# Kernel optimization log

Hardware: AMD Instinct MI355X
Metric: run time of the kernel (lower is better)

The kernel has to match this reference:

```python
import jax, jax.numpy as jnp
import numpy as np

D_MODEL = 96
D_EXP = 192      # d_expand == d_inner (ssm_ratio=ssm_rank_ratio=2)
D_STATE = 16
DT_RANK = 6      # ceil(96/16)
DC_IN = 4        # dc_inner
DC_STATE = 16
DTC_RANK = 6
B, H, W = 2, 48, 48


def _ln_channel(x, w, b):
    # WithBias LayerNorm over channel dim (torch code reshapes b c h w -> b (hw) c)
    mu = x.mean(axis=1, keepdims=True)
    var = ((x - mu) ** 2).mean(axis=1, keepdims=True)
    return (x - mu) / jnp.sqrt(var + 1e-5) * w[None, :, None, None] + b[None, :, None, None]


def _selective_scan(u, delta, A, Bs, Cs, D, delta_bias):
    # u, delta: (b,k,d,l); A: (k,d,n); Bs,Cs: (b,k,n,l); D, delta_bias: (k,d)
    delta = jax.nn.softplus(delta + delta_bias[None, :, :, None])
    dA = jnp.exp(jnp.einsum('bkdl,kdn->bkldn', delta, A))          # decay per step
    dBu = jnp.einsum('bkdl,bkdl,bknl->bkldn', delta, u, Bs)        # input injection

    def combine(c1, c2):
        a1, b1 = c1
        a2, b2 = c2
        return a1 * a2, a2 * b1 + b2

    _, hs = jax.lax.associative_scan(combine, (dA, dBu), axis=2)   # parallel linear recurrence over l
    return jnp.einsum('bkldn,bknl->bkdl', hs, Cs) + D[None, :, :, None] * u


def _spatial_core(x, x_proj_w, dt_w, dt_b, A_logs, Ds, onw, onb):
    b, d, h, w = x.shape
    l = h * w
    # cross_scan_2d: row-major, col-major, and their flips -> (b,4,d,l)
    xs = jnp.stack([x.reshape(b, d, l), jnp.swapaxes(x, 2, 3).reshape(b, d, l)], 1)
    xs = jnp.concatenate([xs, jnp.flip(xs, -1)], 1)
    x_dbl = jnp.einsum('bkdl,kcd->bkcl', xs, x_proj_w)
    dts, Bs, Cs = jnp.split(x_dbl, [DT_RANK, DT_RANK + D_STATE], axis=2)
    dts = jnp.einsum('bkrl,kdr->bkdl', dts, dt_w)
    A = -jnp.exp(A_logs).reshape(4, d, D_STATE)
    out_y = _selective_scan(xs, dts, A, Bs, Cs, Ds.reshape(4, d), dt_b)  # (b,4,d,l)
    inv = jnp.flip(out_y[:, 2:4], -1)
    wh = jnp.swapaxes(out_y[:, 1].reshape(b, d, w, h), 2, 3).reshape(b, d, l)
    invwh = jnp.swapaxes(inv[:, 1].reshape(b, d, w, h), 2, 3).reshape(b, d, l)
    y = (out_y[:, 0] + inv[:, 0] + wh + invwh).reshape(b, d, h, w)
    return _ln_channel(y, onw, onb)


def _channel_core(y, cin_w, cin_b, cout_w, cout_b, xc_proj_w, dtc_w, dtc_b, Ac_logs, Dsc, cnw, cnb):
    b, d = y.shape[0], y.shape[1]
    xc = y.mean(axis=(2, 3))                                              # adaptive avg pool -> (b,d)
    xc = xc[:, None, :] * cin_w.reshape(1, DC_IN, 1) + cin_b.reshape(1, DC_IN, 1)  # 1x1 conv_cin -> (b,4,d)
    xsc = jnp.stack([xc, jnp.flip(xc, -1)], 1)                            # (b,2,dc,L=d)
    xc_dbl = jnp.einsum('bkdl,kcd->bkcl', xsc, xc_proj_w)
    dtsc, Bc, Cc = jnp.split(xc_dbl, [DTC_RANK, DTC_RANK + DC_STATE], axis=2)
    dtsc = jnp.einsum('bkrl,kdr->bkdl', dtsc, dtc_w)
    Ac = -jnp.exp(Ac_logs).reshape(2, DC_IN, DC_STATE)
    outc = _selective_scan(xsc, dtsc, Ac, Bc, Cc, Dsc.reshape(2, DC_IN), dtc_b)  # (b,2,dc,d)
    yc = outc[:, 0] + jnp.flip(outc[:, 1], -1)                            # merge fwd/bwd channel scans
    yc = jnp.einsum('bdl,d->bl', yc, cout_w.reshape(DC_IN)) + cout_b.reshape(())  # 1x1 conv_cout
    return _ln_channel(yc.reshape(b, d, 1, 1), cnw, cnb)


def _conv1x1(x, w, b):
    return jnp.einsum('bchw,oc->bohw', x, w.reshape(w.shape[0], w.shape[1])) + b[None, :, None, None]


def _forward(x, in_w, in_b, dw_w, dw_b, x_proj_w, dt_w, dt_b, A_logs, Ds, out_norm_w, out_norm_b,
             cin_w, cin_b, cout_w, cout_b, xc_proj_w, dtc_w, dtc_b, Ac_logs, Dsc, cn_w, cn_b,
             out_w, out_b):
    xz = _conv1x1(x, in_w, in_b)                      # (b, 2*d_expand, h, w)
    x1, z = xz[:, :D_EXP], xz[:, D_EXP:]
    z = jax.nn.silu(z)
    x1 = jax.lax.conv_general_dilated(x1, dw_w, (1, 1), 'SAME',
                                      dimension_numbers=('NCHW', 'OIHW', 'NCHW'),
                                      feature_group_count=D_EXP) + dw_b[None, :, None, None]
    x1 = jax.nn.silu(x1)
    y = _spatial_core(x1, x_proj_w, dt_w, dt_b, A_logs, Ds, out_norm_w, out_norm_b)
    c = _channel_core(y, cin_w, cin_b, cout_w, cout_b, xc_proj_w, dtc_w, dtc_b, Ac_logs, Dsc, cn_w, cn_b)
    y = y * c * z                                     # channel modulation + gating
    return _conv1x1(y, out_w, out_b)


def setup_inputs():
    key = jax.random.key(0)
    ks = jax.random.split(key, 24)
    s = 0.02

    def rn(k, shape, scale=s):
        return jax.random.normal(k, shape, jnp.float32) * scale

    A_logs = jnp.log(jnp.tile(jnp.arange(1, D_STATE + 1, dtype=jnp.float32)[None, :], (4 * D_EXP, 1)))
    return dict(
        x=jax.random.normal(ks[0], (B, D_MODEL, H, W), jnp.float32),
        in_w=rn(ks[1], (2 * D_EXP, D_MODEL, 1, 1)),
        in_b=rn(ks[2], (2 * D_EXP,)),
        dw_w=rn(ks[3], (D_EXP, 1, 3, 3)),
        dw_b=rn(ks[4], (D_EXP,)),
        x_proj_w=rn(ks[5], (4, DT_RANK + 2 * D_STATE, D_EXP)),
        dt_w=rn(ks[6], (4, D_EXP, DT_RANK), 0.1),
        dt_b=rn(ks[7], (4, D_EXP), 0.5) - 4.0,
        A_logs=A_logs,
        Ds=jnp.ones((4 * D_EXP,), jnp.float32),
        out_norm_w=jnp.ones((D_EXP,), jnp.float32),
        out_norm_b=jnp.zeros((D_EXP,), jnp.float32),
        cin_w=rn(ks[8], (DC_IN, 1, 1, 1), 0.5),
        cin_b=rn(ks[9], (DC_IN,), 0.1),
        cout_w=rn(ks[10], (1, DC_IN, 1, 1), 0.5),
        cout_b=rn(ks[11], (1,), 0.1),
        xc_proj_w=rn(ks[12], (2, DTC_RANK + 2 * DC_STATE, DC_IN), 0.2),
        dtc_w=rn(ks[13], (2, DC_IN, DTC_RANK), 0.2),
        dtc_b=rn(ks[14], (2, DC_IN), 0.5),
        Ac_logs=rn(ks[15], (2 * DC_IN, DC_STATE), 1.0),
        Dsc=jnp.ones((2 * DC_IN,), jnp.float32),
        cn_w=jnp.ones((D_EXP,), jnp.float32),
        cn_b=jnp.zeros((D_EXP,), jnp.float32),
        out_w=rn(ks[16], (D_MODEL, D_EXP, 1, 1)),
        out_b=rn(ks[17], (D_MODEL,)),
    )


def reference(x, in_w, in_b, dw_w, dw_b, x_proj_w, dt_w, dt_b, A_logs, Ds, out_norm_w, out_norm_b,
              cin_w, cin_b, cout_w, cout_b, xc_proj_w, dtc_w, dtc_b, Ac_logs, Dsc, cn_w, cn_b,
              out_w, out_b):
    return _forward(x, in_w, in_b, dw_w, dw_b, x_proj_w, dt_w, dt_b, A_logs, Ds, out_norm_w, out_norm_b,
                    cin_w, cin_b, cout_w, cout_b, xc_proj_w, dtc_w, dtc_b, Ac_logs, Dsc, cn_w, cn_b,
                    out_w, out_b)
```

## Files before the change

### kernel.cpp

```cpp
#include <hip/hip_runtime.h>
#include <math.h>

#define DM 96
#define DE 192
#define LL 2304
#define NS 16
#define RK 6
#define NC 38
#define CH4 64
#define CL4 36

__device__ __forceinline__ float silu_f(float x){ return x / (1.f + __expf(-x)); }
__device__ __forceinline__ float softplus_f(float x){
  return (x > 20.f) ? x : __logf(1.f + __expf(x));
}

__device__ __forceinline__ int dir_map(int k, int l){
    switch(k){
      case 0: return l;
      case 1: return (l % 48) * 48 + l / 48;
      case 2: return 2303 - l;
      default: { int lr = 2303 - l; return (lr % 48) * 48 + lr / 48; }
    }
}

__global__ __launch_bounds__(384) void k1_conv_in(const float* __restrict__ x,
    const float* __restrict__ in_w, const float* __restrict__ in_b,
    float* __restrict__ x1raw, float* __restrict__ z){
  __shared__ float xv[DM*16];
  int tile = blockIdx.x;
  int b = tile / 144;
  int pos0 = (tile % 144) * 16;
  int tid = threadIdx.x;
  {
    int c = tid >> 2, p4 = tid & 3;
    float4 v = *(const float4*)(x + (b*DM + c)*LL + pos0 + p4*4);
    *(float4*)&xv[c*16 + p4*4] = v;
  }
  __syncthreads();
  float acc[16];
  #pragma unroll
  for (int p=0;p<16;p++) acc[p] = in_b[tid];
  const float4* wv4 = (const float4*)(in_w + tid*DM);
  #pragma unroll 4
  for (int c4=0;c4<24;c4++){
    float4 wv = wv4[c4];
    #pragma unroll
    for (int cc=0;cc<4;cc++){
      float w = (cc==0)?wv.x:((cc==1)?wv.y:((cc==2)?wv.z:wv.w));
      const float* xr = &xv[(c4*4+cc)*16];
      #pragma unroll
      for (int p4=0;p4<4;p4++){
        float4 xq = *(const float4*)&xr[p4*4];
        acc[p4*4+0] = fmaf(w, xq.x, acc[p4*4+0]);
        acc[p4*4+1] = fmaf(w, xq.y, acc[p4*4+1]);
        acc[p4*4+2] = fmaf(w, xq.z, acc[p4*4+2]);
        acc[p4*4+3] = fmaf(w, xq.w, acc[p4*4+3]);
      }
    }
  }
  if (tid < DE){
    float* dst = x1raw + (b*DE + tid)*LL + pos0;
    #pragma unroll
    for (int p4=0;p4<4;p4++)
      *(float4*)(dst + p4*4) = make_float4(acc[p4*4+0],acc[p4*4+1],acc[p4*4+2],acc[p4*4+3]);
  } else {
    int zc = tid - DE;
    float* dst = z + (b*DE + zc)*LL + pos0;
    #pragma unroll
    for (int p4=0;p4<4;p4++)
      *(float4*)(dst + p4*4) = make_float4(silu_f(acc[p4*4+0]),silu_f(acc[p4*4+1]),
                                           silu_f(acc[p4*4+2]),silu_f(acc[p4*4+3]));
  }
}

__global__ __launch_bounds__(256) void k2_dwconv(const float* __restrict__ x1raw,
    const float* __restrict__ dw_w, const float* __restrict__ dw_b,
    float* __restrict__ xconv, float* __restrict__ xconvT){
  __shared__ float lin[50][52];
  __shared__ float lout[48][50];
  int bd = blockIdx.x;
  int d = bd % DE;
  int tid = threadIdx.x;
  for (int i = tid; i < 50*52; i += 256) ((float*)lin)[i] = 0.f;
  __syncthreads();
  const float* src = x1raw + bd*LL;
  for (int i = tid; i < 576; i += 256){
    int r = i/12, c4 = (i%12)*4;
    float4 v = *(const float4*)(src + r*48 + c4);
    lin[r+1][c4+1] = v.x; lin[r+1][c4+2] = v.y; lin[r+1][c4+3] = v.z; lin[r+1][c4+4] = v.w;
  }
  float w00=dw_w[d*9+0], w01=dw_w[d*9+1], w02=dw_w[d*9+2];
  float w10=dw_w[d*9+3], w11=dw_w[d*9+4], w12=dw_w[d*9+5];
  float w20=dw_w[d*9+6], w21=dw_w[d*9+7], w22=dw_w[d*9+8];
  float bias = dw_b[d];
  __syncthreads();
  float* dst = xconv + bd*LL;
  for (int i = tid; i < 576; i += 256){
    int h = i/12, w4 = (i%12)*4;
    float o[4];
    #pragma unroll
    for (int j=0;j<4;j++){
      int w = w4 + j;
      float acc = bias;
      acc = fmaf(w00, lin[h  ][w], fmaf(w01, lin[h  ][w+1], fmaf(w02, lin[h  ][w+2], acc)));
      acc = fmaf(w10, lin[h+1][w], fmaf(w11, lin[h+1][w+1], fmaf(w12, lin[h+1][w+2], acc)));
      acc = fmaf(w20, lin[h+2][w], fmaf(w21, lin[h+2][w+1], fmaf(w22, lin[h+2][w+2], acc)));
      float v = silu_f(acc);
      o[j] = v;
      lout[h][w] = v;
    }
    *(float4*)(dst + h*48 + w4) = make_float4(o[0],o[1],o[2],o[3]);
  }
  __syncthreads();
  float* dstT = xconvT + bd*LL;
  for (int i = tid; i < 576; i += 256){
    int tw = i/12, th4 = (i%12)*4;
    float4 v = make_float4(lout[th4][tw], lout[th4+1][tw], lout[th4+2][tw], lout[th4+3][tw]);
    *(float4*)(dstT + tw*48 + th4) = v;
  }
}

__global__ __launch_bounds__(256) void k3_proj(const float* __restrict__ xconv,
    const float* __restrict__ xconvT,
    const float* __restrict__ x_proj_w, const float* __restrict__ dt_w,
    const float* __restrict__ dt_b, float* __restrict__ delta,
    float* __restrict__ Bs, float* __restrict__ Cs){
  __shared__ float smem[38*256];
  int bk = blockIdx.x / 36;
  int tile = blockIdx.x % 36;
  int b = bk >> 2, k = bk & 3;
  int tid = threadIdx.x;
  int lsub = tid & 63, dgrp = tid >> 6;
  int l = tile*64 + lsub;
  const float* wsrc = x_proj_w + k*NC*DE;
  for (int idx = tid; idx < NC*DE; idx += 256){
    int c = idx / DE, d = idx % DE;
    smem[d*40 + c] = wsrc[idx];
  }
  if (tid < DE){ smem[tid*40 + 38] = 0.f; smem[tid*40 + 39] = 0.f; }
  __syncthreads();
  float acc[40];
  #pragma unroll
  for (int c=0;c<40;c++) acc[c]=0.f;
  const float* uptr;
  {
    const float* basep = (k & 1) ? (xconvT + b*DE*LL) : (xconv + b*DE*LL);
    uptr = basep + ((k >= 2) ? (2303 - l) : l);
  }
  for (int dd=0; dd<48; dd++){
    int d = dgrp*48 + dd;
    float u = uptr[d*LL];
    const float4* wrow = (const float4*)&smem[d*40];
    #pragma unroll
    for (int j=0;j<10;j++){
      float4 wv = wrow[j];
      acc[j*4+0] = fmaf(u, wv.x, acc[j*4+0]);
      acc[j*4+1] = fmaf(u, wv.y, acc[j*4+1]);
      acc[j*4+2] = fmaf(u, wv.z, acc[j*4+2]);
      acc[j*4+3] = fmaf(u, wv.w, acc[j*4+3]);
    }
  }
  __syncthreads();
  #pragma unroll
  for (int c=0;c<38;c++) smem[c*256 + dgrp*64 + lsub] = acc[c];
  __syncthreads();
  for (int idx = tid; idx < 38*64; idx += 256){
    int c = idx >> 6, l2 = idx & 63;
    float s = smem[c*256 + l2] + smem[c*256 + 64 + l2]
            + smem[c*256 + 128 + l2] + smem[c*256 + 192 + l2];
    int lg = tile*64 + l2;
    if (c < RK){
      smem[c*256 + l2] = s;
    } else if (c < RK + NS){
      Bs[(bk*LL + lg)*NS + (c - RK)] = s;
    } else {
      Cs[(bk*LL + lg)*NS + (c - RK - NS)] = s;
    }
  }
  __syncthreads();
  float r0 = smem[0*256 + lsub], r1 = smem[1*256 + lsub], r2 = smem[2*256 + lsub];
  float r3 = smem[3*256 + lsub], r4 = smem[4*256 + lsub], r5 = smem[5*256 + lsub];
  const float* dwb = dt_w + k*DE*RK;
  const float* dbb = dt_b + k*DE;
  for (int dd=0; dd<48; dd++){
    int d = dgrp*48 + dd;
    const float* wr = dwb + d*RK;
    float t = dbb[d];
    t = fmaf(r0, wr[0], t); t = fmaf(r1, wr[1], t); t = fmaf(r2, wr[2], t);
    t = fmaf(r3, wr[3], t); t = fmaf(r4, wr[4], t); t = fmaf(r5, wr[5], t);
    delta[(bk*DE + d)*LL + l] = softplus_f(t);
  }
}

__global__ __launch_bounds__(256) void k4_scan(const float* __restrict__ xconv,
    const float* __restrict__ xconvT,
    const float* __restrict__ delta, const float* __restrict__ Bs,
    const float* __restrict__ Cs, const float* __restrict__ A_logs,
    const float* __restrict__ Ds, float* __restrict__ out_y){
  int gid = blockIdx.x;
  int b = gid / (4*DE);
  int kd = gid % (4*DE);
  int k = kd / DE;
  int d = kd % DE;
  int bk = b*4 + k;
  int tid = threadIdx.x;
  int c = tid >> 2, q = tid & 3;
  const float LOG2E = 1.44269504f;
  float4 al = *(const float4*)&A_logs[(k*DE + d)*NS + q*4];
  float A2[4];
  A2[0] = -__expf(al.x)*LOG2E; A2[1] = -__expf(al.y)*LOG2E;
  A2[2] = -__expf(al.z)*LOG2E; A2[3] = -__expf(al.w)*LOG2E;
  float Dv = Ds[k*DE + d];
  const float* dptr = delta + (bk*DE + d)*LL;
  const float* ub = ((k & 1) ? xconvT : xconv) + (b*DE + d)*LL;
  bool rev = (k >= 2);
  const float* bbase = Bs + bk*LL*NS + q*4;
  const float* cbase = Cs + bk*LL*NS + q*4;
  float* optr = out_y + (bk*DE + d)*LL;
  int l0 = c*CL4;
  float sumdl = 0.f, S[4] = {0.f,0.f,0.f,0.f};
  #pragma unroll 3
  for (int i=0;i<CL4;i+=4){
    int l = l0 + i;
    float4 dl4 = *(const float4*)(dptr + l);
    float4 u4;
    if (!rev) u4 = *(const float4*)(ub + l);
    else { float4 t = *(const float4*)(ub + (LL-4) - l); u4 = make_float4(t.w,t.z,t.y,t.x); }
    #pragma unroll
    for (int j=0;j<4;j++){
      float dlj = (j==0)?dl4.x:((j==1)?dl4.y:((j==2)?dl4.z:dl4.w));
      float uj  = (j==0)?u4.x:((j==1)?u4.y:((j==2)?u4.z:u4.w));
      float du = dlj*uj;
      sumdl += dlj;
      float4 Bv = *(const float4*)(bbase + (l+j)*NS);
      float dA0 = exp2f(dlj*A2[0]); S[0] = fmaf(S[0], dA0, du*Bv.x);
      float dA1 = exp2f(dlj*A2[1]); S[1] = fmaf(S[1], dA1, du*Bv.y);
      float dA2 = exp2f(dlj*A2[2]); S[2] = fmaf(S[2], dA2, du*Bv.z);
      float dA3 = exp2f(dlj*A2[3]); S[3] = fmaf(S[3], dA3, du*Bv.w);
    }
  }
  __shared__ float sP[CH4][NS], sS[CH4][NS];
  __shared__ float oy[LL];
  *(float4*)&sP[c][q*4] = make_float4(exp2f(A2[0]*sumdl), exp2f(A2[1]*sumdl),
                                      exp2f(A2[2]*sumdl), exp2f(A2[3]*sumdl));
  *(float4*)&sS[c][q*4] = make_float4(S[0],S[1],S[2],S[3]);
  __syncthreads();
  if (tid < NS){
    float hacc = 0.f;
    #pragma unroll 4
    for (int cc=0; cc<CH4; cc++){
      hacc = fmaf(hacc, sP[cc][tid], sS[cc][tid]);
      sS[cc][tid] = hacc;
    }
  }
  __syncthreads();
  float h[4];
  if (c == 0){ h[0]=h[1]=h[2]=h[3]=0.f; }
  else { float4 hi = *(const float4*)&sS[c-1][q*4]; h[0]=hi.x; h[1]=hi.y; h[2]=hi.z; h[3]=hi.w; }
  #pragma unroll 3
  for (int i=0;i<CL4;i+=4){
    int l = l0 + i;
    float4 dl4 = *(const float4*)(dptr + l);
    float4 u4;
    if (!rev) u4 = *(const float4*)(ub + l);
    else { float4 t = *(const float4*)(ub + (LL-4) - l); u4 = make_float4(t.w,t.z,t.y,t.x); }
    #pragma unroll
    for (int j=0;j<4;j++){
      float dlj = (j==0)?dl4.x:((j==1)?dl4.y:((j==2)?dl4.z:dl4.w));
      float uj  = (j==0)?u4.x:((j==1)?u4.y:((j==2)?u4.z:u4.w));
      float du = dlj*uj;
      float4 Bv = *(const float4*)(bbase + (l+j)*NS);
      float4 Cv = *(const float4*)(cbase + (l+j)*NS);
      float dA0 = exp2f(dlj*A2[0]); h[0] = fmaf(h[0], dA0, du*Bv.x);
      float dA1 = exp2f(dlj*A2[1]); h[1] = fmaf(h[1], dA1, du*Bv.y);
      float dA2 = exp2f(dlj*A2[2]); h[2] = fmaf(h[2], dA2, du*Bv.z);
      float dA3 = exp2f(dlj*A2[3]); h[3] = fmaf(h[3], dA3, du*Bv.w);
      float py = h[0]*Cv.x + h[1]*Cv.y + h[2]*Cv.z + h[3]*Cv.w;
      py += __shfl_xor(py, 1);
      py += __shfl_xor(py, 2);
      if (q == 0){
        oy[dir_map(k, l+j)] = fmaf(Dv, uj, py);
      }
    }
  }
  __syncthreads();
  {
    float4* o4 = (float4*)optr;
    const float4* s4 = (const float4*)oy;
    for (int i = tid; i < LL/4; i += 256) o4[i] = s4[i];
  }
}

__global__ __launch_bounds__(256) void k5_combine_ln(const float* __restrict__ out_y,
    const float* __restrict__ onw, const float* __restrict__ onb,
    float* __restrict__ y_ln, float* __restrict__ partial){
  __shared__ float vals[DE][17];
  __shared__ float s_[16][16], s2_[16][16];
  __shared__ float mu_[16], rs_[16];
  int bT = blockIdx.x;
  int b = bT / 144;
  int pos0 = (bT % 144) * 16;
  int tid = threadIdx.x;
  int p = tid & 15, g = tid >> 4;
  const float* base = out_y + b*4*DE*LL;
  float s = 0.f, s2 = 0.f;
  #pragma unroll
  for (int j=0;j<12;j++){
    int d = g*12 + j;
    int idx = d*LL + pos0 + p;
    float v = base[idx] + base[DE*LL + idx] + base[2*DE*LL + idx] + base[3*DE*LL + idx];
    vals[d][p] = v;
    s += v; s2 += v*v;
  }
  s_[g][p] = s; s2_[g][p] = s2;
  __syncthreads();
  if (tid < 16){
    float ss = 0.f, ss2 = 0.f;
    #pragma unroll
    for (int gg=0; gg<16; gg++){ ss += s_[gg][tid]; ss2 += s2_[gg][tid]; }
    float mu = ss / DE;
    float var = ss2 / DE - mu*mu;
    mu_[tid] = mu; rs_[tid] = rsqrtf(var + 1e-5f);
  }
  __syncthreads();
  float mu = mu_[p], rs = rs_[p];
  #pragma unroll
  for (int j=0;j<12;j++){
    int d = g*12 + j;
    float yv = (vals[d][p] - mu)*rs*onw[d] + onb[d];
    y_ln[(b*DE + d)*LL + pos0 + p] = yv;
    vals[d][p] = yv;
  }
  __syncthreads();
  if (tid < DE){
    float ps = 0.f;
    #pragma unroll
    for (int pp=0;pp<16;pp++) ps += vals[tid][pp];
    partial[bT*DE + tid] = ps;
  }
}

__global__ __launch_bounds__(512) void k6b_channel(const float* __restrict__ partial,
    const float* __restrict__ cin_w, const float* __restrict__ cin_b,
    const float* __restrict__ cout_w, const float* __restrict__ cout_b,
    const float* __restrict__ xc_proj_w, const float* __restrict__ dtc_w,
    const float* __restrict__ dtc_b, const float* __restrict__ Ac_logs,
    const float* __restrict__ Dsc, const float* __restrict__ cn_w,
    const float* __restrict__ cn_b, float* __restrict__ cvec){
  __shared__ float xcs[DE];
  __shared__ float tmp[384];
  __shared__ float sP[128][4], sS[128][4];
  __shared__ float outc[2][4][DE];
  __shared__ float ycs[DE];
  __shared__ float muS, rsS;
  int b = blockIdx.x;
  int tid = threadIdx.x;
  if (tid < 384){
    int d = tid % DE, half = tid / DE;
    const float* pp = partial + (b*144 + half*72)*DE + d;
    float sacc = 0.f;
    #pragma unroll 8
    for (int t=0;t<72;t++) sacc += pp[t*DE];
    tmp[tid] = sacc;
  }
  __syncthreads();
  if (tid < DE) xcs[tid] = (tmp[tid] + tmp[tid + DE]) * (1.f/LL);
  __syncthreads();
  int chain = tid >> 2, ch = tid & 3;
  int k = chain >> 6, dc = (chain >> 4) & 3, n = chain & 15;
  const float LOG2E = 1.44269504f;
  float EW0=0,EW1=0,EW2=0,EW3=0;
  #pragma unroll
  for (int r=0;r<RK;r++){
    float dw = dtc_w[(k*4+dc)*RK + r];
    EW0 = fmaf(dw, xc_proj_w[(k*NC + r)*4 + 0], EW0);
    EW1 = fmaf(dw, xc_proj_w[(k*NC + r)*4 + 1], EW1);
    EW2 = fmaf(dw, xc_proj_w[(k*NC + r)*4 + 2], EW2);
    EW3 = fmaf(dw, xc_proj_w[(k*NC + r)*4 + 3], EW3);
  }
  float Bw0 = xc_proj_w[(k*NC + RK + n)*4 + 0];
  float Bw1 = xc_proj_w[(k*NC + RK + n)*4 + 1];
  float Bw2 = xc_proj_w[(k*NC + RK + n)*4 + 2];
  float Bw3 = xc_proj_w[(k*NC + RK + n)*4 + 3];
  float Cw0 = xc_proj_w[(k*NC + RK + NS + n)*4 + 0];
  float Cw1 = xc_proj_w[(k*NC + RK + NS + n)*4 + 1];
  float Cw2 = xc_proj_w[(k*NC + RK + NS + n)*4 + 2];
  float Cw3 = xc_proj_w[(k*NC + RK + NS + n)*4 + 3];
  float A2 = -__expf(Ac_logs[(k*4+dc)*NS + n]) * LOG2E;
  float Dv = Dsc[k*4+dc];
  float dtb = dtc_b[k*4+dc];
  float ciw0=cin_w[0], ciw1=cin_w[1], ciw2=cin_w[2], ciw3=cin_w[3];
  float cib0=cin_b[0], cib1=cin_b[1], cib2=cin_b[2], cib3=cin_b[3];
  int l0 = ch*48;
  float P = 1.f, S = 0.f;
  for (int i=0;i<48;i++){
    int lc = l0 + i;
    int lp = k ? (191 - lc) : lc;
    float xv = xcs[lp];
    float xs0 = fmaf(xv, ciw0, cib0);
    float xs1 = fmaf(xv, ciw1, cib1);
    float xs2 = fmaf(xv, ciw2, cib2);
    float xs3 = fmaf(xv, ciw3, cib3);
    float dt = dtb + xs0*EW0 + xs1*EW1 + xs2*EW2 + xs3*EW3;
    float dl = softplus_f(dt);
    float Bv = xs0*Bw0 + xs1*Bw1 + xs2*Bw2 + xs3*Bw3;
    float u = (dc==0)?xs0:((dc==1)?xs1:((dc==2)?xs2:xs3));
    float dA = exp2f(dl * A2);
    S = fmaf(S, dA, dl*u*Bv);
    P *= dA;
  }
  sP[chain][ch] = P; sS[chain][ch] = S;
  __syncthreads();
  if (tid < 128){
    float hacc = 0.f;
    #pragma unroll
    for (int cc=0; cc<4; cc++){
      hacc = fmaf(hacc, sP[tid][cc], sS[tid][cc]);
      sS[tid][cc] = hacc;
    }
  }
  __syncthreads();
  float h = (ch == 0) ? 0.f : sS[chain][ch-1];
  for (int i=0;i<48;i++){
    int lc = l0 + i;
    int lp = k ? (191 - lc) : lc;
    float xv = xcs[lp];
    float xs0 = fmaf(xv, ciw0, cib0);
    float xs1 = fmaf(xv, ciw1, cib1);
    float xs2 = fmaf(xv, ciw2, cib2);
    float xs3 = fmaf(xv, ciw3, cib3);
    float dt = dtb + xs0*EW0 + xs1*EW1 + xs2*EW2 + xs3*EW3;
    float dl = softplus_f(dt);
    float Bv = xs0*Bw0 + xs1*Bw1 + xs2*Bw2 + xs3*Bw3;
    float Cv = xs0*Cw0 + xs1*Cw1 + xs2*Cw2 + xs3*Cw3;
    float u = (dc==0)?xs0:((dc==1)?xs1:((dc==2)?xs2:xs3));
    float dA = exp2f(dl * A2);
    h = fmaf(h, dA, dl*u*Bv);
    float py = h * Cv;
    py += __shfl_xor(py, 4);
    py += __shfl_xor(py, 8);
    py += __shfl_xor(py, 16);
    py += __shfl_xor(py, 32);
    if (n == 0) outc[k][dc][lc] = fmaf(Dv, u, py);
  }
  __syncthreads();
  float co0=cout_w[0], co1=cout_w[1], co2=cout_w[2], co3=cout_w[3], cob=cout_b[0];
  for (int i = tid; i < DE; i += 512){
    float yv = cob
      + co0*(outc[0][0][i] + outc[1][0][191-i])
      + co1*(outc[0][1][i] + outc[1][1][191-i])
      + co2*(outc[0][2][i] + outc[1][2][191-i])
      + co3*(outc[0][3][i] + outc[1][3][191-i]);
    ycs[i] = yv;
  }
  __syncthreads();
  if (tid < 64){
    float s = 0.f, s2 = 0.f;
    #pragma unroll
    for (int j=0;j<3;j++){
      float v = ycs[tid + j*64];
      s += v; s2 += v*v;
    }
    for (int off=32; off>0; off>>=1){ s += __shfl_down(s, off); s2 += __shfl_down(s2, off); }
    if (tid == 0){
      float mu = s / DE;
      float var = s2 / DE - mu*mu;
      muS = mu; rsS = rsqrtf(var + 1e-5f);
    }
  }
  __syncthreads();
  float mu = muS, rs = rsS;
  for (int i = tid; i < DE; i += 512){
    cvec[b*DE + i] = (ycs[i] - mu) * rs * cn_w[i] + cn_b[i];
  }
}

__global__ __launch_bounds__(256) void k7_out(const float* __restrict__ y_ln,
    const float* __restrict__ cvec, const float* __restrict__ z,
    const float* __restrict__ out_w, const float* __restrict__ out_b,
    float* __restrict__ outp){
  __shared__ float t[DE*16];
  int tile = blockIdx.x;
  int b = tile / 144;
  int pos0 = (tile % 144) * 16;
  int tid = threadIdx.x;
  for (int i = tid; i < DE*4; i += 256){
    int c = i >> 2, p4 = (i & 3)*4;
    int gi = (b*DE + c)*LL + pos0 + p4;
    float4 yv = *(const float4*)(y_ln + gi);
    float4 zv = *(const float4*)(z + gi);
    float cv = cvec[b*DE + c];
    *(float4*)&t[c*16 + p4] = make_float4(yv.x*cv*zv.x, yv.y*cv*zv.y, yv.z*cv*zv.z, yv.w*cv*zv.w);
  }
  __syncthreads();
  for (int j = tid; j < DM*16; j += 256){
    int o = j >> 4, p = j & 15;
    float acc = out_b[o];
    const float4* wr4 = (const float4*)(out_w + o*DE);
    #pragma unroll 8
    for (int c4=0;c4<48;c4++){
      float4 wv = wr4[c4];
      acc = fmaf(wv.x, t[(c4*4+0)*16+p], acc);
      acc = fmaf(wv.y, t[(c4*4+1)*16+p], acc);
      acc = fmaf(wv.z, t[(c4*4+2)*16+p], acc);
      acc = fmaf(wv.w, t[(c4*4+3)*16+p], acc);
    }
    outp[(b*DM + o)*LL + pos0 + p] = acc;
  }
}

extern "C" void kernel_launch(void* const* d_in, const int* in_sizes, int n_in,
                              void* d_out, int out_size, void* d_ws, size_t ws_size,
                              hipStream_t stream){
  const float* x        = (const float*)d_in[0];
  const float* in_w     = (const float*)d_in[1];
  const float* in_b     = (const float*)d_in[2];
  const float* dw_w     = (const float*)d_in[3];
  const float* dw_b     = (const float*)d_in[4];
  const float* x_proj_w = (const float*)d_in[5];
  const float* dt_w     = (const float*)d_in[6];
  const float* dt_b     = (const float*)d_in[7];
  const float* A_logs   = (const float*)d_in[8];
  const float* Ds       = (const float*)d_in[9];
  const float* onw      = (const float*)d_in[10];
  const float* onb      = (const float*)d_in[11];
  const float* cin_w    = (const float*)d_in[12];
  const float* cin_b    = (const float*)d_in[13];
  const float* cout_w   = (const float*)d_in[14];
  const float* cout_b   = (const float*)d_in[15];
  const float* xc_proj_w= (const float*)d_in[16];
  const float* dtc_w    = (const float*)d_in[17];
  const float* dtc_b    = (const float*)d_in[18];
  const float* Ac_logs  = (const float*)d_in[19];
  const float* Dsc      = (const float*)d_in[20];
  const float* cn_w     = (const float*)d_in[21];
  const float* cn_b     = (const float*)d_in[22];
  const float* out_w    = (const float*)d_in[23];
  const float* out_b    = (const float*)d_in[24];

  float* ws = (float*)d_ws;
  float* x1raw = ws;  ws += 2*DE*LL;
  float* zbuf  = ws;  ws += 2*DE*LL;
  float* xconv = ws;  ws += 2*DE*LL;
  float* delta = ws;  ws += 2*4*DE*LL;
  float* Bsb   = ws;  ws += 2*4*LL*NS;
  float* Csb   = ws;  ws += 2*4*LL*NS;
  float* outy  = ws;  ws += 2*4*DE*LL;
  float* yln   = ws;  ws += 2*DE*LL;
  float* cvec  = ws;  ws += 2*DE;
  float* partial = ws; ws += 2*144*DE;
  float* xconvT = yln;

  hipLaunchKernelGGL(k1_conv_in, dim3(288), dim3(384), 0, stream, x, in_w, in_b, x1raw, zbuf);
  hipLaunchKernelGGL(k2_dwconv, dim3(384), dim3(256), 0, stream, x1raw, dw_w, dw_b, xconv, xconvT);
  hipLaunchKernelGGL(k3_proj, dim3(288), dim3(256), 0, stream, xconv, xconvT, x_proj_w, dt_w, dt_b, delta, Bsb, Csb);
  hipLaunchKernelGGL(k4_scan, dim3(1536), dim3(256), 0, stream, xconv, xconvT, delta, Bsb, Csb, A_logs, Ds, outy);
  hipLaunchKernelGGL(k5_combine_ln, dim3(288), dim3(256), 0, stream, outy, onw, onb, yln, partial);
  hipLaunchKernelGGL(k6b_channel, dim3(2), dim3(512), 0, stream, partial, cin_w, cin_b, cout_w, cout_b,
                     xc_proj_w, dtc_w, dtc_b, Ac_logs, Dsc, cn_w, cn_b, cvec);
  hipLaunchKernelGGL(k7_out, dim3(288), dim3(256), 0, stream, yln, cvec, zbuf, out_w, out_b, (float*)d_out);
}
```

Measured before the change: 185.6 us.

## Fuse four scan directions per block and defer LayerNorm apply to output kernel

The scan kernel now runs all four directions for one (batch, channel) in a single 1024-thread block and sums them in shared memory, writing one combined tensor instead of four per-direction outputs. The LayerNorm pass is split: a stats kernel writes per-position mean and rstd plus normalized partial sums, and the output projection kernel applies the norm inline. This cuts global traffic from writing and re-reading the four-direction out_y and the y_ln buffer. In exchange the scan uses larger blocks with 36KB of shared memory, which may lower occupancy, and adds an extra barrier.

```diff
diff --git a/kernel.cpp b/kernel.cpp
--- a/kernel.cpp
+++ b/kernel.cpp
@@ -193,19 +193,23 @@
   }
 }
 
-__global__ __launch_bounds__(256) void k4_scan(const float* __restrict__ xconv,
+__global__ __launch_bounds__(1024) void k4_scan(const float* __restrict__ xconv,
     const float* __restrict__ xconvT,
     const float* __restrict__ delta, const float* __restrict__ Bs,
     const float* __restrict__ Cs, const float* __restrict__ A_logs,
-    const float* __restrict__ Ds, float* __restrict__ out_y){
+    const float* __restrict__ Ds, float* __restrict__ ycomb){
+  __shared__ float smem4[4*LL];
+  float* sPf = smem4;
+  float* sSf = smem4 + 4096;
+  float* oyf = smem4;
   int gid = blockIdx.x;
-  int b = gid / (4*DE);
-  int kd = gid % (4*DE);
-  int k = kd / DE;
-  int d = kd % DE;
+  int b = gid / DE;
+  int d = gid % DE;
+  int tid = threadIdx.x;
+  int k = tid >> 8;
+  int sub = tid & 255;
+  int c = sub >> 2, q = sub & 3;
   int bk = b*4 + k;
-  int tid = threadIdx.x;
-  int c = tid >> 2, q = tid & 3;
   const float LOG2E = 1.44269504f;
   float4 al = *(const float4*)&A_logs[(k*DE + d)*NS + q*4];
   float A2[4];
@@ -217,7 +221,6 @@
   bool rev = (k >= 2);
   const float* bbase = Bs + bk*LL*NS + q*4;
   const float* cbase = Cs + bk*LL*NS + q*4;
-  float* optr = out_y + (bk*DE + d)*LL;
   int l0 = c*CL4;
   float sumdl = 0.f, S[4] = {0.f,0.f,0.f,0.f};
   #pragma unroll 3
@@ -240,24 +243,27 @@
       float dA3 = exp2f(dlj*A2[3]); S[3] = fmaf(S[3], dA3, du*Bv.w);
     }
   }
-  __shared__ float sP[CH4][NS], sS[CH4][NS];
-  __shared__ float oy[LL];
-  *(float4*)&sP[c][q*4] = make_float4(exp2f(A2[0]*sumdl), exp2f(A2[1]*sumdl),
-                                      exp2f(A2[2]*sumdl), exp2f(A2[3]*sumdl));
-  *(float4*)&sS[c][q*4] = make_float4(S[0],S[1],S[2],S[3]);
-  __syncthreads();
-  if (tid < NS){
+  *(float4*)&sPf[(k*CH4 + c)*NS + q*4] = make_float4(exp2f(A2[0]*sumdl), exp2f(A2[1]*sumdl),
+                                                     exp2f(A2[2]*sumdl), exp2f(A2[3]*sumdl));
+  *(float4*)&sSf[(k*CH4 + c)*NS + q*4] = make_float4(S[0],S[1],S[2],S[3]);
+  __syncthreads();
+  if (sub < NS){
     float hacc = 0.f;
     #pragma unroll 4
     for (int cc=0; cc<CH4; cc++){
-      hacc = fmaf(hacc, sP[cc][tid], sS[cc][tid]);
-      sS[cc][tid] = hacc;
+      int idx = (k*CH4 + cc)*NS + sub;
+      hacc = fmaf(hacc, sPf[idx], sSf[idx]);
+      sSf[idx] = hacc;
     }
   }
   __syncthreads();
   float h[4];
   if (c == 0){ h[0]=h[1]=h[2]=h[3]=0.f; }
-  else { float4 hi = *(const float4*)&sS[c-1][q*4]; h[0]=hi.x; h[1]=hi.y; h[2]=hi.z; h[3]=hi.w; }
+  else {
+    float4 hi = *(const float4*)&sSf[(k*CH4 + c-1)*NS + q*4];
+    h[0]=hi.x; h[1]=hi.y; h[2]=hi.z; h[3]=hi.w;
+  }
+  __syncthreads();
   #pragma unroll 3
   for (int i=0;i<CL4;i+=4){
     int l = l0 + i;
@@ -280,21 +286,28 @@
       py += __shfl_xor(py, 1);
       py += __shfl_xor(py, 2);
       if (q == 0){
-        oy[dir_map(k, l+j)] = fmaf(Dv, uj, py);
+        oyf[k*LL + dir_map(k, l+j)] = fmaf(Dv, uj, py);
       }
     }
   }
   __syncthreads();
   {
-    float4* o4 = (float4*)optr;
-    const float4* s4 = (const float4*)oy;
-    for (int i = tid; i < LL/4; i += 256) o4[i] = s4[i];
-  }
-}
-
-__global__ __launch_bounds__(256) void k5_combine_ln(const float* __restrict__ out_y,
-    const float* __restrict__ onw, const float* __restrict__ onb,
-    float* __restrict__ y_ln, float* __restrict__ partial){
+    float4* o4 = (float4*)(ycomb + (b*DE + d)*LL);
+    const float4* s0 = (const float4*)(oyf);
+    const float4* s1 = (const float4*)(oyf + LL);
+    const float4* s2 = (const float4*)(oyf + 2*LL);
+    const float4* s3 = (const float4*)(oyf + 3*LL);
+    for (int i = tid; i < LL/4; i += 1024){
+      float4 a = s0[i], e = s1[i], f = s2[i], g = s3[i];
+      o4[i] = make_float4(a.x+e.x+f.x+g.x, a.y+e.y+f.y+g.y,
+                          a.z+e.z+f.z+g.z, a.w+e.w+f.w+g.w);
+    }
+  }
+}
+
+__global__ __launch_bounds__(256) void k5_stats(const float* __restrict__ ycomb,
+    float* __restrict__ mu_g, float* __restrict__ rs_g,
+    float* __restrict__ partial){
   __shared__ float vals[DE][17];
   __shared__ float s_[16][16], s2_[16][16];
   __shared__ float mu_[16], rs_[16];
@@ -303,13 +316,12 @@
   int pos0 = (bT % 144) * 16;
   int tid = threadIdx.x;
   int p = tid & 15, g = tid >> 4;
-  const float* base = out_y + b*4*DE*LL;
+  const float* base = ycomb + b*DE*LL;
   float s = 0.f, s2 = 0.f;
   #pragma unroll
   for (int j=0;j<12;j++){
     int d = g*12 + j;
-    int idx = d*LL + pos0 + p;
-    float v = base[idx] + base[DE*LL + idx] + base[2*DE*LL + idx] + base[3*DE*LL + idx];
+    float v = base[d*LL + pos0 + p];
     vals[d][p] = v;
     s += v; s2 += v*v;
   }
@@ -322,26 +334,20 @@
     float mu = ss / DE;
     float var = ss2 / DE - mu*mu;
     mu_[tid] = mu; rs_[tid] = rsqrtf(var + 1e-5f);
-  }
-  __syncthreads();
-  float mu = mu_[p], rs = rs_[p];
-  #pragma unroll
-  for (int j=0;j<12;j++){
-    int d = g*12 + j;
-    float yv = (vals[d][p] - mu)*rs*onw[d] + onb[d];
-    y_ln[(b*DE + d)*LL + pos0 + p] = yv;
-    vals[d][p] = yv;
+    mu_g[b*LL + pos0 + tid] = mu;
+    rs_g[b*LL + pos0 + tid] = rs_[tid];
   }
   __syncthreads();
   if (tid < DE){
     float ps = 0.f;
     #pragma unroll
-    for (int pp=0;pp<16;pp++) ps += vals[tid][pp];
+    for (int pp=0;pp<16;pp++) ps += (vals[tid][pp] - mu_[pp]) * rs_[pp];
     partial[bT*DE + tid] = ps;
   }
 }
 
 __global__ __launch_bounds__(512) void k6b_channel(const float* __restrict__ partial,
+    const float* __restrict__ onw, const float* __restrict__ onb,
     const float* __restrict__ cin_w, const float* __restrict__ cin_b,
     const float* __restrict__ cout_w, const float* __restrict__ cout_b,
     const float* __restrict__ xc_proj_w, const float* __restrict__ dtc_w,
@@ -365,7 +371,7 @@
     tmp[tid] = sacc;
   }
   __syncthreads();
-  if (tid < DE) xcs[tid] = (tmp[tid] + tmp[tid + DE]) * (1.f/LL);
+  if (tid < DE) xcs[tid] = fmaf(onw[tid], (tmp[tid] + tmp[tid + DE]) * (1.f/LL), onb[tid]);
   __syncthreads();
   int chain = tid >> 2, ch = tid & 3;
   int k = chain >> 6, dc = (chain >> 4) & 3, n = chain & 15;
@@ -476,7 +482,9 @@
   }
 }
 
-__global__ __launch_bounds__(256) void k7_out(const float* __restrict__ y_ln,
+__global__ __launch_bounds__(256) void k7_out(const float* __restrict__ ycomb,
+    const float* __restrict__ mu_g, const float* __restrict__ rs_g,
+    const float* __restrict__ onw, const float* __restrict__ onb,
     const float* __restrict__ cvec, const float* __restrict__ z,
     const float* __restrict__ out_w, const float* __restrict__ out_b,
     float* __restrict__ outp){
@@ -488,10 +496,17 @@
   for (int i = tid; i < DE*4; i += 256){
     int c = i >> 2, p4 = (i & 3)*4;
     int gi = (b*DE + c)*LL + pos0 + p4;
-    float4 yv = *(const float4*)(y_ln + gi);
+    float4 yv = *(const float4*)(ycomb + gi);
     float4 zv = *(const float4*)(z + gi);
+    float4 m4 = *(const float4*)(mu_g + b*LL + pos0 + p4);
+    float4 r4 = *(const float4*)(rs_g + b*LL + pos0 + p4);
+    float w = onw[c], bb = onb[c];
     float cv = cvec[b*DE + c];
-    *(float4*)&t[c*16 + p4] = make_float4(yv.x*cv*zv.x, yv.y*cv*zv.y, yv.z*cv*zv.z, yv.w*cv*zv.w);
+    float t0 = fmaf((yv.x - m4.x)*r4.x, w, bb) * cv * zv.x;
+    float t1 = fmaf((yv.y - m4.y)*r4.y, w, bb) * cv * zv.y;
+    float t2 = fmaf((yv.z - m4.z)*r4.z, w, bb) * cv * zv.z;
+    float t3 = fmaf((yv.w - m4.w)*r4.w, w, bb) * cv * zv.w;
+    *(float4*)&t[c*16 + p4] = make_float4(t0,t1,t2,t3);
   }
   __syncthreads();
   for (int j = tid; j < DM*16; j += 256){
@@ -543,21 +558,22 @@
   float* x1raw = ws;  ws += 2*DE*LL;
   float* zbuf  = ws;  ws += 2*DE*LL;
   float* xconv = ws;  ws += 2*DE*LL;
+  float* xconvT= ws;  ws += 2*DE*LL;
   float* delta = ws;  ws += 2*4*DE*LL;
   float* Bsb   = ws;  ws += 2*4*LL*NS;
   float* Csb   = ws;  ws += 2*4*LL*NS;
-  float* outy  = ws;  ws += 2*4*DE*LL;
-  float* yln   = ws;  ws += 2*DE*LL;
+  float* ycomb = ws;  ws += 2*DE*LL;
   float* cvec  = ws;  ws += 2*DE;
   float* partial = ws; ws += 2*144*DE;
-  float* xconvT = yln;
+  float* mu_g  = ws;  ws += 2*LL;
+  float* rs_g  = ws;  ws += 2*LL;
 
   hipLaunchKernelGGL(k1_conv_in, dim3(288), dim3(384), 0, stream, x, in_w, in_b, x1raw, zbuf);
   hipLaunchKernelGGL(k2_dwconv, dim3(384), dim3(256), 0, stream, x1raw, dw_w, dw_b, xconv, xconvT);
   hipLaunchKernelGGL(k3_proj, dim3(288), dim3(256), 0, stream, xconv, xconvT, x_proj_w, dt_w, dt_b, delta, Bsb, Csb);
-  hipLaunchKernelGGL(k4_scan, dim3(1536), dim3(256), 0, stream, xconv, xconvT, delta, Bsb, Csb, A_logs, Ds, outy);
-  hipLaunchKernelGGL(k5_combine_ln, dim3(288), dim3(256), 0, stream, outy, onw, onb, yln, partial);
-  hipLaunchKernelGGL(k6b_channel, dim3(2), dim3(512), 0, stream, partial, cin_w, cin_b, cout_w, cout_b,
+  hipLaunchKernelGGL(k4_scan, dim3(384), dim3(1024), 0, stream, xconv, xconvT, delta, Bsb, Csb, A_logs, Ds, ycomb);
+  hipLaunchKernelGGL(k5_stats, dim3(288), dim3(256), 0, stream, ycomb, mu_g, rs_g, partial);
+  hipLaunchKernelGGL(k6b_channel, dim3(2), dim3(512), 0, stream, partial, onw, onb, cin_w, cin_b, cout_w, cout_b,
                      xc_proj_w, dtc_w, dtc_b, Ac_logs, Dsc, cn_w, cn_b, cvec);
-  hipLaunchKernelGGL(k7_out, dim3(288), dim3(256), 0, stream, yln, cvec, zbuf, out_w, out_b, (float*)d_out);
-}
+  hipLaunchKernelGGL(k7_out, dim3(288), dim3(256), 0, stream, ycomb, mu_g, rs_g, onw, onb, cvec, zbuf, out_w, out_b, (float*)d_out);
+}
```

New measurement: 192.6 us. +3.8%, slower.
